# Kernel optimization log

Measured on AMD Instinct MI355X. Metric: run time of the kernel, lower is better.

Reference implementation:

```python
import jax, jax.numpy as jnp
import numpy as np
from jax import lax

KH, KW = 3, 3
KK = KH * KW
PAD = 1  # 'same' padding for 3x3, stride 1, dilation 1


def setup_inputs() -> dict:
    key = jax.random.key(0)
    k1, k2, k3 = jax.random.split(key, 3)
    B, H, W, C, F = 8, 64, 64, 128, 128
    x = jax.random.normal(k1, (B, H, W, C), dtype=jnp.float32)
    # glorot-ish scale for main kernel; small scale for offset predictor so
    # sampled offsets are a few pixels (original zero-inits offsets; random
    # small values exercise the bilinear path).
    kernel = jax.random.normal(k2, (KH, KW, C, F), dtype=jnp.float32) * 0.05
    bias = jnp.zeros((F,), dtype=jnp.float32)
    offset_w = jax.random.normal(k3, (KH, KW, C, 2 * KK), dtype=jnp.float32) * 0.01
    offset_b = jnp.zeros((2 * KK,), dtype=jnp.float32)
    return {"x": x, "kernel": kernel, "bias": bias,
            "offset_w": offset_w, "offset_b": offset_b}


def _deform_conv(x, kernel, bias, offset_w, offset_b):
    B, H, W, C = x.shape
    F = kernel.shape[-1]

    # 1) offset-predicting conv, 'same' padding -> [B,H,W,2*KK]
    offsets = lax.conv_general_dilated(
        x, offset_w, window_strides=(1, 1), padding='SAME',
        dimension_numbers=('NHWC', 'HWIO', 'NHWC')) + offset_b
    offsets = offsets.reshape(B, H, W, KK, 2)
    dy, dx = offsets[..., 0], offsets[..., 1]  # [B,H,W,KK]

    # 2) sampling positions: base grid + kernel tap offset + learned offset
    ky = jnp.repeat(jnp.arange(KH, dtype=jnp.float32) - PAD, KW)  # [KK]
    kx = jnp.tile(jnp.arange(KW, dtype=jnp.float32) - PAD, KH)    # [KK]
    py = jnp.arange(H, dtype=jnp.float32)[None, :, None, None] + ky + dy  # [B,H,W,KK]
    px = jnp.arange(W, dtype=jnp.float32)[None, None, :, None] + kx + dx

    # 3) bilinear sampling with zero padding outside the image
    y0 = jnp.floor(py)
    x0 = jnp.floor(px)
    wy = py - y0  # [B,H,W,KK]
    wx = px - x0
    y0i = y0.astype(jnp.int32)
    x0i = x0.astype(jnp.int32)
    b_idx = jnp.arange(B)[:, None, None, None]

    def gather(yi, xi):
        valid = (yi >= 0) & (yi < H) & (xi >= 0) & (xi < W)
        yc = jnp.clip(yi, 0, H - 1)
        xc = jnp.clip(xi, 0, W - 1)
        v = x[b_idx, yc, xc]  # [B,H,W,KK,C]
        return v * valid[..., None].astype(x.dtype)

    val = (gather(y0i, x0i) * ((1 - wy) * (1 - wx))[..., None]
           + gather(y0i, x0i + 1) * ((1 - wy) * wx)[..., None]
           + gather(y0i + 1, x0i) * (wy * (1 - wx))[..., None]
           + gather(y0i + 1, x0i + 1) * (wy * wx)[..., None])  # [B,H,W,KK,C]

    # 4) convolution weighted sum over taps and input channels
    out = jnp.einsum('bhwkc,kcf->bhwf', val, kernel.reshape(KK, C, F))
    return out + bias


def reference(x, kernel, bias, offset_w, offset_b):
    return _deform_conv(x, kernel, bias, offset_w, offset_b)
```

## Files before the change

kernel.cpp:

```cpp
#include <hip/hip_runtime.h>

#define BB 8
#define HH 64
#define WW 64
#define CC 128
#define FF 128

typedef __attribute__((ext_vector_type(8))) short short8v;
typedef __attribute__((ext_vector_type(4))) float float4v;

#define MFMA(a, b, c) __builtin_amdgcn_mfma_f32_16x16x32_bf16((a), (b), (c), 0, 0, 0)

__device__ __forceinline__ ushort f2bf(float f) {
    uint u = __float_as_uint(f);
    u += 0x7FFF + ((u >> 16) & 1);
    return (ushort)(u >> 16);
}
__device__ __forceinline__ float bf2f(ushort h) {
    return __uint_as_float(((uint)h) << 16);
}

#define OFFS_BYTES (BB * HH * WW * 18 * 2)
#define NFRAG_MAIN (36 * 8 * 64)
#define NFRAG_OFF  (36 * 2 * 64)

__global__ __launch_bounds__(256)
void prep_weights(const float* __restrict__ kern, const float* __restrict__ offw,
                  ushort* __restrict__ wfrag, ushort* __restrict__ ofrag)
{
    int idx = blockIdx.x * 256 + threadIdx.x;
    if (idx < NFRAG_MAIN) {
        const int ks = idx >> 9;
        const int nt = (idx >> 6) & 7;
        const int l  = idx & 63;
        const int tap = ks >> 2;
        const int f   = nt * 16 + (l & 15);
        const int c0  = (ks & 3) * 32 + 8 * (l >> 4);
        uint p[4];
#pragma unroll
        for (int j2 = 0; j2 < 4; ++j2) {
            const ushort h0 = f2bf(kern[(tap * CC + c0 + 2 * j2) * FF + f]);
            const ushort h1 = f2bf(kern[(tap * CC + c0 + 2 * j2 + 1) * FF + f]);
            p[j2] = (uint)h0 | ((uint)h1 << 16);
        }
        *(uint4*)(wfrag + idx * 8) = make_uint4(p[0], p[1], p[2], p[3]);
    } else if (idx < NFRAG_MAIN + NFRAG_OFF) {
        idx -= NFRAG_MAIN;
        const int ks = idx >> 7;
        const int nt = (idx >> 6) & 1;
        const int l  = idx & 63;
        const int tap = ks >> 2;
        const int o   = nt * 16 + (l & 15);
        const int c0  = (ks & 3) * 32 + 8 * (l >> 4);
        uint p[4];
#pragma unroll
        for (int j2 = 0; j2 < 4; ++j2) {
            const float v0 = (o < 18) ? offw[(tap * CC + c0 + 2 * j2) * 18 + o] : 0.f;
            const float v1 = (o < 18) ? offw[(tap * CC + c0 + 2 * j2 + 1) * 18 + o] : 0.f;
            p[j2] = (uint)f2bf(v0) | ((uint)f2bf(v1) << 16);
        }
        *(uint4*)(ofrag + idx * 8) = make_uint4(p[0], p[1], p[2], p[3]);
    }
}

__global__ __launch_bounds__(256)
void offsets_mfma(const float* __restrict__ x, const ushort* __restrict__ ofrag,
                  const float* __restrict__ ob, ushort* __restrict__ offs_out)
{
    const int bid  = blockIdx.x;
    const int swzb = (bid & 7) * 64 + (bid >> 3);
    const int b = swzb >> 6, h = swzb & 63;
    const int tid = threadIdx.x, l = tid & 63, w = tid >> 6;
    const int row = l & 15, kb = l >> 4;
    const int px  = w * 16 + row;

    const float* xb = x + b * HH * WW * CC;
    const short8v* OF = (const short8v*)ofrag;

    float4v acc0 = {0.f, 0.f, 0.f, 0.f};
    float4v acc1 = {0.f, 0.f, 0.f, 0.f};

    for (int ks = 0; ks < 36; ++ks) {
        const int tap = ks >> 2;
        const int ky = tap / 3 - 1, kx = tap % 3 - 1;
        const int y = h + ky;
        if ((unsigned)y >= (unsigned)HH) continue;
        const int xc = px + kx;
        const int c0 = (ks & 3) * 32 + kb * 8;

        float4 v0 = make_float4(0.f, 0.f, 0.f, 0.f);
        float4 v1 = make_float4(0.f, 0.f, 0.f, 0.f);
        if ((unsigned)xc < (unsigned)WW) {
            const float* p = xb + (y * WW + xc) * CC + c0;
            v0 = *(const float4*)p;
            v1 = *(const float4*)(p + 4);
        }
        short8v ah;
        ah[0] = (short)f2bf(v0.x); ah[1] = (short)f2bf(v0.y);
        ah[2] = (short)f2bf(v0.z); ah[3] = (short)f2bf(v0.w);
        ah[4] = (short)f2bf(v1.x); ah[5] = (short)f2bf(v1.y);
        ah[6] = (short)f2bf(v1.z); ah[7] = (short)f2bf(v1.w);

        acc0 = MFMA(ah, OF[(ks * 2 + 0) * 64 + l], acc0);
        acc1 = MFMA(ah, OF[(ks * 2 + 1) * 64 + l], acc1);
    }

    ushort* og = offs_out + (b * HH + h) * WW * 18;
#pragma unroll
    for (int nt = 0; nt < 2; ++nt) {
        const int o = nt * 16 + (l & 15);
        if (o < 18) {
            const float bo = ob[o];
            const float4v a = nt ? acc1 : acc0;
#pragma unroll
            for (int r = 0; r < 4; ++r) {
                const int ppx = w * 16 + kb * 4 + r;
                og[ppx * 18 + o] = f2bf(a[r] + bo);
            }
        }
    }
}

__device__ __forceinline__ float4 corner_load(const float* __restrict__ xb,
                                              int yi, int xi, int c4)
{
    if ((unsigned)yi < (unsigned)HH && (unsigned)xi < (unsigned)WW)
        return *(const float4*)(xb + (yi * WW + xi) * CC + c4);
    return make_float4(0.f, 0.f, 0.f, 0.f);
}

__global__ __launch_bounds__(256)
void deform_direct(const float* __restrict__ x, const ushort* __restrict__ wfrag,
                   const float* __restrict__ bias, const ushort* __restrict__ offs_g,
                   float* __restrict__ out)
{
    const int bid  = blockIdx.x;
    const int swzb = (bid & 7) * 64 + (bid >> 3);
    const int b = swzb >> 6, h = swzb & 63;
    const int tid = threadIdx.x, l = tid & 63, w = tid >> 6;
    const int row = l & 15, kb = l >> 4;
    const int px  = w * 16 + row;

    const float* xb = x + b * HH * WW * CC;
    const ushort* og = offs_g + ((b * HH + h) * WW + px) * 18;
    const short8v* WF = (const short8v*)wfrag;

    float4v acc[8];
#pragma unroll
    for (int nt = 0; nt < 8; ++nt) acc[nt] = (float4v){0.f, 0.f, 0.f, 0.f};

    for (int tap = 0; tap < 9; ++tap) {
        const int ky = tap / 3 - 1, kx = tap % 3 - 1;
        const uint dyx = *(const uint*)(og + 2 * tap);
        const float dy = bf2f((ushort)(dyx & 0xFFFFu));
        const float dx = bf2f((ushort)(dyx >> 16));
        const float py  = (float)(h + ky) + dy;
        const float pxf = (float)(px + kx) + dx;
        const float y0f = floorf(py), x0f = floorf(pxf);
        const float wy = py - y0f, wx = pxf - x0f;
        const int yi = (int)y0f, xi = (int)x0f;
        const float w00 = (1.f - wy) * (1.f - wx);
        const float w01 = (1.f - wy) * wx;
        const float w10 = wy * (1.f - wx);
        const float w11 = wy * wx;

#pragma unroll
        for (int ks2 = 0; ks2 < 4; ++ks2) {
            const int c0 = ks2 * 32 + kb * 8;
            const float4 a00 = corner_load(xb, yi,     xi,     c0);
            const float4 b00 = corner_load(xb, yi,     xi,     c0 + 4);
            const float4 a01 = corner_load(xb, yi,     xi + 1, c0);
            const float4 b01 = corner_load(xb, yi,     xi + 1, c0 + 4);
            const float4 a10 = corner_load(xb, yi + 1, xi,     c0);
            const float4 b10 = corner_load(xb, yi + 1, xi,     c0 + 4);
            const float4 a11 = corner_load(xb, yi + 1, xi + 1, c0);
            const float4 b11 = corner_load(xb, yi + 1, xi + 1, c0 + 4);

            float v[8];
            v[0] = a00.x * w00 + a01.x * w01 + a10.x * w10 + a11.x * w11;
            v[1] = a00.y * w00 + a01.y * w01 + a10.y * w10 + a11.y * w11;
            v[2] = a00.z * w00 + a01.z * w01 + a10.z * w10 + a11.z * w11;
            v[3] = a00.w * w00 + a01.w * w01 + a10.w * w10 + a11.w * w11;
            v[4] = b00.x * w00 + b01.x * w01 + b10.x * w10 + b11.x * w11;
            v[5] = b00.y * w00 + b01.y * w01 + b10.y * w10 + b11.y * w11;
            v[6] = b00.z * w00 + b01.z * w01 + b10.z * w10 + b11.z * w11;
            v[7] = b00.w * w00 + b01.w * w01 + b10.w * w10 + b11.w * w11;

            short8v ah;
#pragma unroll
            for (int j = 0; j < 8; ++j) ah[j] = (short)f2bf(v[j]);

            const int fb = ((tap * 4 + ks2) * 8) * 64 + l;
#pragma unroll
            for (int nt = 0; nt < 8; ++nt)
                acc[nt] = MFMA(ah, WF[fb + nt * 64], acc[nt]);
        }
    }

    float* ob_ = out + ((b * HH + h) * WW + w * 16) * FF;
#pragma unroll
    for (int nt = 0; nt < 8; ++nt) {
        const int f = nt * 16 + (l & 15);
        const float bv = bias[f];
#pragma unroll
        for (int r = 0; r < 4; ++r) {
            const int opx = kb * 4 + r;
            ob_[opx * FF + f] = acc[nt][r] + bv;
        }
    }
}

extern "C" void kernel_launch(void* const* d_in, const int* in_sizes, int n_in,
                              void* d_out, int out_size, void* d_ws, size_t ws_size,
                              hipStream_t stream)
{
    (void)in_sizes; (void)n_in; (void)out_size; (void)ws_size;
    const float* x    = (const float*)d_in[0];
    const float* kern = (const float*)d_in[1];
    const float* bias = (const float*)d_in[2];
    const float* ow   = (const float*)d_in[3];
    const float* ob   = (const float*)d_in[4];
    float* outp = (float*)d_out;

    char* ws = (char*)d_ws;
    ushort* offs  = (ushort*)ws;
    ushort* wfrag = (ushort*)(ws + OFFS_BYTES);
    ushort* ofrag = (ushort*)(ws + OFFS_BYTES + 294912);

    const int prep_threads = NFRAG_MAIN + NFRAG_OFF;
    prep_weights<<<(prep_threads + 255) / 256, 256, 0, stream>>>(kern, ow, wfrag, ofrag);
    offsets_mfma<<<BB * HH, 256, 0, stream>>>(x, ofrag, ob, offs);
    deform_direct<<<BB * HH, 256, 0, stream>>>(x, wfrag, bias, offs, outp);
}
```

Before: 179.9 us.

## Split deformable conv taps across two wave groups with LDS reduction

Doubles the block to 512 threads, with two groups of four waves each taking a subset of the 9 taps (4 and 5) for the same 64 pixels. The partial accumulators are combined through shared memory before the bias add and store. It also prefetches the next tap's offsets. The aim is more waves in flight to hide the latency of the bilinear gathers. The cost is a __syncthreads, an LDS round-trip, an uneven split between the groups, and a tighter register budget from launch_bounds(512,4).

```diff
diff --git a/kernel.cpp b/kernel.cpp
--- a/kernel.cpp
+++ b/kernel.cpp
@@ -129,17 +129,21 @@
     return make_float4(0.f, 0.f, 0.f, 0.f);
 }
 
-__global__ __launch_bounds__(256)
+__global__ __launch_bounds__(512, 4)
 void deform_direct(const float* __restrict__ x, const ushort* __restrict__ wfrag,
                    const float* __restrict__ bias, const ushort* __restrict__ offs_g,
                    float* __restrict__ out)
 {
+    __shared__ float4 lds_red[8 * 4 * 64];
+
     const int bid  = blockIdx.x;
     const int swzb = (bid & 7) * 64 + (bid >> 3);
     const int b = swzb >> 6, h = swzb & 63;
-    const int tid = threadIdx.x, l = tid & 63, w = tid >> 6;
+    const int tid = threadIdx.x, l = tid & 63, wv = tid >> 6;
+    const int g = wv >> 2;
+    const int t = wv & 3;
     const int row = l & 15, kb = l >> 4;
-    const int px  = w * 16 + row;
+    const int px  = t * 16 + row;
 
     const float* xb = x + b * HH * WW * CC;
     const ushort* og = offs_g + ((b * HH + h) * WW + px) * 18;
@@ -149,9 +153,16 @@
 #pragma unroll
     for (int nt = 0; nt < 8; ++nt) acc[nt] = (float4v){0.f, 0.f, 0.f, 0.f};
 
-    for (int tap = 0; tap < 9; ++tap) {
+    const int tap_begin = g ? 4 : 0;
+    const int tap_end   = g ? 9 : 4;
+
+    uint dyx_next = *(const uint*)(og + 2 * tap_begin);
+#pragma unroll 1
+    for (int tap = tap_begin; tap < tap_end; ++tap) {
+        const uint dyx = dyx_next;
+        if (tap + 1 < tap_end) dyx_next = *(const uint*)(og + 2 * (tap + 1));
+
         const int ky = tap / 3 - 1, kx = tap % 3 - 1;
-        const uint dyx = *(const uint*)(og + 2 * tap);
         const float dy = bf2f((ushort)(dyx & 0xFFFFu));
         const float dx = bf2f((ushort)(dyx >> 16));
         const float py  = (float)(h + ky) + dy;
@@ -197,15 +208,26 @@
         }
     }
 
-    float* ob_ = out + ((b * HH + h) * WW + w * 16) * FF;
-#pragma unroll
-    for (int nt = 0; nt < 8; ++nt) {
-        const int f = nt * 16 + (l & 15);
-        const float bv = bias[f];
-#pragma unroll
-        for (int r = 0; r < 4; ++r) {
-            const int opx = kb * 4 + r;
-            ob_[opx * FF + f] = acc[nt][r] + bv;
+    if (g == 1) {
+#pragma unroll
+        for (int nt = 0; nt < 8; ++nt)
+            lds_red[(nt * 4 + t) * 64 + l] =
+                make_float4(acc[nt][0], acc[nt][1], acc[nt][2], acc[nt][3]);
+    }
+    __syncthreads();
+    if (g == 0) {
+        float* ob_ = out + ((b * HH + h) * WW + t * 16) * FF;
+#pragma unroll
+        for (int nt = 0; nt < 8; ++nt) {
+            const int f = nt * 16 + (l & 15);
+            const float bv = bias[f];
+            const float4 p = lds_red[(nt * 4 + t) * 64 + l];
+            const float pr[4] = {p.x, p.y, p.z, p.w};
+#pragma unroll
+            for (int r = 0; r < 4; ++r) {
+                const int opx = kb * 4 + r;
+                ob_[opx * FF + f] = acc[nt][r] + pr[r] + bv;
+            }
         }
     }
 }
@@ -230,5 +252,5 @@
     const int prep_threads = NFRAG_MAIN + NFRAG_OFF;
     prep_weights<<<(prep_threads + 255) / 256, 256, 0, stream>>>(kern, ow, wfrag, ofrag);
     offsets_mfma<<<BB * HH, 256, 0, stream>>>(x, ofrag, ob, offs);
-    deform_direct<<<BB * HH, 256, 0, stream>>>(x, wfrag, bias, offs, outp);
-}
+    deform_direct<<<BB * HH, 512, 0, stream>>>(x, wfrag, bias, offs, outp);
+}
```

New measurement: 174.7 us. 1.03x faster.
